# Kernel tuning notes

Hardware: AMD Instinct MI355X
Metric: run time of the kernel (lower is better)

## Reference

```python
import jax, jax.numpy as jnp
import numpy as np

B, SEQ, PRED, CIN, COUT = 4, 3584, 512, 7, 7
L = SEQ + PRED              # 4096, divisible by 2*BS -> fit_length is a no-op
D, H, DH, FF, EL = 512, 8, 64, 2048, 2
BS, NHASH = 64, 4           # bucket_size, n_hashes
NB = L // BS                # 64 buckets per hash round
SELF_ATTN_VAL = -5e4        # reformer_pytorch TOKEN_SELF_ATTN_VALUE


def layer_norm(x, g, b, eps=1e-5):
    m = jnp.mean(x, -1, keepdims=True)
    v = jnp.mean((x - m) ** 2, -1, keepdims=True)
    return (x - m) * jax.lax.rsqrt(v + eps) * g + b


def lsh_attention(qk, v, rot):
    # qk, v: (bh, L, DH); rot: (DH, NHASH, NB//2)  (shared across batch & heads)
    bh, Lx, dh = qk.shape
    nb = Lx // BS
    # --- hash vectors ---
    rv = jnp.einsum('btf,fhi->bhti', qk, rot)              # (bh, NHASH, L, nb//2)
    rv = jnp.concatenate([rv, -rv], axis=-1)
    buckets = jnp.argmax(rv, axis=-1)                      # (bh, NHASH, L) int
    buckets = buckets + (jnp.arange(NHASH) * nb)[None, :, None]
    buckets = buckets.reshape(bh, NHASH * Lx)
    ticker = jnp.arange(NHASH * Lx)
    bt = Lx * buckets + (ticker % Lx)[None]                # unique keys
    # --- sort by (bucket, position) ---
    sticker = jnp.argsort(bt, axis=-1)                     # (bh, NHASH*L)
    undo = jnp.argsort(sticker, axis=-1)
    st = sticker % Lx
    sqk = jnp.take_along_axis(qk, st[..., None], axis=1)   # (bh, NHASH*L, DH)
    sv = jnp.take_along_axis(v, st[..., None], axis=1)
    ch = NHASH * nb                                        # number of chunks
    bq_t = st.reshape(bh, ch, BS)
    bqk = sqk.reshape(bh, ch, BS, dh)
    bv = sv.reshape(bh, ch, BS, dh)
    bq = bqk
    nrm = jnp.sqrt(jnp.sum(bqk * bqk, -1, keepdims=True))
    bk = bqk / jnp.maximum(nrm, 1e-12)                     # F.normalize
    def look_one_back(t):
        prev = jnp.concatenate([t[:, -1:], t[:, :-1]], axis=1)
        return jnp.concatenate([t, prev], axis=2)
    bk = look_one_back(bk)
    bvv = look_one_back(bv)
    bkv_t = look_one_back(bq_t)
    dots = jnp.einsum('bcie,bcje->bcij', bq, bk) * (dh ** -0.5)  # (bh, ch, BS, 2BS)
    self_mask = bq_t[..., :, None] == bkv_t[..., None, :]
    dots = jnp.where(self_mask, SELF_ATTN_VAL, dots)
    lse = jax.scipy.special.logsumexp(dots, axis=-1, keepdims=True)
    p = jnp.exp(dots - lse)
    bo = jnp.einsum('bcij,bcje->bcie', p, bvv)
    so = bo.reshape(bh, NHASH * Lx, dh)
    slog = lse.reshape(bh, NHASH * Lx)
    o = jnp.take_along_axis(so, undo[..., None], axis=1)
    logits = jnp.take_along_axis(slog, undo, axis=1)
    o = o.reshape(bh, NHASH, Lx, dh)
    logits = logits.reshape(bh, NHASH, Lx, 1)
    probs = jnp.exp(logits - jax.scipy.special.logsumexp(logits, axis=1, keepdims=True))
    return jnp.sum(o * probs, axis=1)                      # (bh, L, DH)


def lsh_self_attention(x, Wqk, Wv, Wo, bo, rot):
    Bs, Lx, _ = x.shape
    qk = (x @ Wqk).reshape(Bs, Lx, H, DH).transpose(0, 2, 1, 3).reshape(Bs * H, Lx, DH)
    v = (x @ Wv).reshape(Bs, Lx, H, DH).transpose(0, 2, 1, 3).reshape(Bs * H, Lx, DH)
    out = lsh_attention(qk, v, rot)
    out = out.reshape(Bs, H, Lx, DH).transpose(0, 2, 1, 3).reshape(Bs, Lx, D)
    return out @ Wo + bo


def _forward(x_enc, x_dec, x_mark_enc, x_mark_dec, conv_w, month_emb, day_emb,
             weekday_emb, hour_emb, minute_emb, W_qk, W_v, W_out, b_out, rotations,
             ln1_g, ln1_b, W_ff1, b_ff1, W_ff2, b_ff2, ln2_g, ln2_b, lnf_g, lnf_b,
             W_proj, b_proj):
    x = jnp.concatenate([x_enc, x_dec[:, -PRED:, :]], axis=1)            # (B, L, CIN)
    xm = jnp.concatenate([x_mark_enc, x_mark_dec[:, -PRED:, :]], axis=1)
    # TokenEmbedding: Conv1d k=3, circular padding, no bias
    xp = jnp.concatenate([x[:, -1:], x, x[:, :1]], axis=1)
    tok = jax.lax.conv_general_dilated(xp, conv_w, (1,), 'VALID',
                                       dimension_numbers=('NWC', 'WIO', 'NWC'))
    # TemporalEmbedding (freq='t': month/day/weekday/hour/minute)
    temp = (month_emb[xm[..., 0]] + day_emb[xm[..., 1]] + weekday_emb[xm[..., 2]]
            + hour_emb[xm[..., 3]] + minute_emb[xm[..., 4]])
    # PositionalEmbedding (sinusoidal)
    pos = jnp.arange(L, dtype=jnp.float32)[:, None]
    div = jnp.exp(jnp.arange(0, D, 2, dtype=jnp.float32) * (-np.log(10000.0) / D))
    pe = jnp.zeros((L, D), jnp.float32).at[:, 0::2].set(jnp.sin(pos * div)).at[:, 1::2].set(jnp.cos(pos * div))
    h = tok + temp + pe[None]
    for l in range(EL):
        a = lsh_self_attention(h, W_qk[l], W_v[l], W_out[l], b_out[l], rotations[l])
        h = layer_norm(h + a, ln1_g[l], ln1_b[l])
        y = jax.nn.gelu(h @ W_ff1[l] + b_ff1[l], approximate=False)
        y = y @ W_ff2[l] + b_ff2[l]
        h = layer_norm(h + y, ln2_g[l], ln2_b[l])
    h = layer_norm(h, lnf_g, lnf_b)
    return h[:, -PRED:] @ W_proj + b_proj                  # (B, PRED, COUT)


def setup_inputs():
    ks = jax.random.split(jax.random.key(0), 20)
    def n(k, shape, fan_in):
        return jax.random.normal(k, shape, jnp.float32) / np.sqrt(fan_in)
    return {
        'x_enc': jax.random.normal(ks[0], (B, SEQ, CIN), jnp.float32),
        'x_dec': jax.random.normal(ks[1], (B, PRED, CIN), jnp.float32),
        'x_mark_enc': jax.random.randint(ks[2], (B, SEQ, 5), 0, 4, jnp.int32),
        'x_mark_dec': jax.random.randint(ks[3], (B, PRED, 5), 0, 4, jnp.int32),
        'conv_w': n(ks[4], (3, CIN, D), 3 * CIN),
        'month_emb': 0.02 * jax.random.normal(ks[5], (13, D), jnp.float32),
        'day_emb': 0.02 * jax.random.normal(ks[6], (32, D), jnp.float32),
        'weekday_emb': 0.02 * jax.random.normal(ks[7], (7, D), jnp.float32),
        'hour_emb': 0.02 * jax.random.normal(ks[8], (24, D), jnp.float32),
        'minute_emb': 0.02 * jax.random.normal(ks[9], (4, D), jnp.float32),
        'W_qk': n(ks[10], (EL, D, D), D),
        'W_v': n(ks[11], (EL, D, D), D),
        'W_out': n(ks[12], (EL, D, D), D),
        'b_out': jnp.zeros((EL, D), jnp.float32),
        'rotations': jax.random.normal(ks[13], (EL, DH, NHASH, NB // 2), jnp.float32),
        'ln1_g': jnp.ones((EL, D), jnp.float32),
        'ln1_b': jnp.zeros((EL, D), jnp.float32),
        'W_ff1': n(ks[14], (EL, D, FF), D),
        'b_ff1': jnp.zeros((EL, FF), jnp.float32),
        'W_ff2': n(ks[15], (EL, FF, D), FF),
        'b_ff2': jnp.zeros((EL, D), jnp.float32),
        'ln2_g': jnp.ones((EL, D), jnp.float32),
        'ln2_b': jnp.zeros((EL, D), jnp.float32),
        'lnf_g': jnp.ones((D,), jnp.float32),
        'lnf_b': jnp.zeros((D,), jnp.float32),
        'W_proj': n(ks[16], (D, COUT), D),
        'b_proj': jnp.zeros((COUT,), jnp.float32),
    }


def reference(x_enc, x_dec, x_mark_enc, x_mark_dec, conv_w, month_emb, day_emb,
              weekday_emb, hour_emb, minute_emb, W_qk, W_v, W_out, b_out, rotations,
              ln1_g, ln1_b, W_ff1, b_ff1, W_ff2, b_ff2, ln2_g, ln2_b, lnf_g, lnf_b,
              W_proj, b_proj):
    return _forward(x_enc, x_dec, x_mark_enc, x_mark_dec, conv_w, month_emb, day_emb,
                    weekday_emb, hour_emb, minute_emb, W_qk, W_v, W_out, b_out, rotations,
                    ln1_g, ln1_b, W_ff1, b_ff1, W_ff2, b_ff2, ln2_g, ln2_b, lnf_g, lnf_b,
                    W_proj, b_proj)
```

## Files before the change

kernel.cpp:

```cpp
#include <hip/hip_runtime.h>
#include <math.h>


typedef __attribute__((ext_vector_type(8))) __bf16 bf16x8;
typedef __attribute__((ext_vector_type(4))) float floatx4;

__device__ __forceinline__ unsigned short f2bf(float f) {
  union { float f; unsigned int u; } x; x.f = f;
  unsigned int r = x.u + 0x7fffu + ((x.u >> 16) & 1u);
  return (unsigned short)(r >> 16);
}
__device__ __forceinline__ float bf2f(unsigned short u) {
  union { unsigned int u; float f; } x; x.u = ((unsigned int)u) << 16;
  return x.f;
}
__device__ __forceinline__ float gelu_f(float x) {
  return 0.5f * x * (1.0f + erff(x * 0.70710678118654752440f));
}

__global__ __launch_bounds__(256) void pe_kernel(float* __restrict__ pe)
{
  int t = blockIdx.x;
#pragma unroll
  for (int rep = 0; rep < 2; ++rep) {
    int d = threadIdx.x + rep * 256;
    float cf = (float)(-9.210340371976184 / 512.0);
    float xf = (float)(d & ~1) * cf;
    float freq = (float)exp((double)xf);
    float angf = (float)t * freq;
    double a = (double)angf;
    pe[t * 512 + d] = (float)((d & 1) ? cos(a) : sin(a));
  }
}

__global__ __launch_bounds__(256) void embed_kernel(
    const float* __restrict__ x_enc, const float* __restrict__ x_dec,
    const int* __restrict__ xm_enc, const int* __restrict__ xm_dec,
    const float* __restrict__ conv_w,
    const float* __restrict__ month, const float* __restrict__ day,
    const float* __restrict__ wday, const float* __restrict__ hour,
    const float* __restrict__ minute, const float* __restrict__ pe,
    float* __restrict__ h)
{
  int idx = blockIdx.x;
  int b = idx >> 12, t = idx & 4095;
  __shared__ float xv[21];
  __shared__ int mi[5];
  int tid = threadIdx.x;
  if (tid < 21) {
    int w = tid / 7, c = tid % 7;
    int s = (t + w + 4095) & 4095;
    xv[tid] = (s < 3584) ? x_enc[(s + b*3584)*7 + c]
                         : x_dec[((s - 3584) + b*512)*7 + c];
  }
  if (tid >= 32 && tid < 37) {
    int j = tid - 32;
    mi[j] = (t < 3584) ? xm_enc[(b*3584 + t)*5 + j]
                       : xm_dec[(b*512 + (t - 3584))*5 + j];
  }
  __syncthreads();
  int m0 = mi[0], m1 = mi[1], m2 = mi[2], m3 = mi[3], m4 = mi[4];
#pragma unroll
  for (int rep = 0; rep < 2; ++rep) {
    int d = tid + rep*256;
    float tok = 0.f;
#pragma unroll
    for (int wc = 0; wc < 21; ++wc) tok += xv[wc] * conv_w[wc*512 + d];
    float temp = month[m0*512+d] + day[m1*512+d] + wday[m2*512+d]
               + hour[m3*512+d] + minute[m4*512+d];
    h[(size_t)idx*512 + d] = tok + temp + pe[t*512 + d];
  }
}

template<int ACT>
__global__ __launch_bounds__(256) void gemm_kernel(
    const float* __restrict__ A, const float* __restrict__ W,
    const float* __restrict__ bias, float* __restrict__ C,
    int M, int N, int K)
{
  __shared__ float As[8][132];
  __shared__ float Bs[8][132];
  int tid = threadIdx.x;
  int bm = blockIdx.x, bn = blockIdx.y;
  int tr = tid >> 4, tc = tid & 15;
  double acc[8][8];
  float tt[8][8];
#pragma unroll
  for (int i=0;i<8;++i)
#pragma unroll
    for (int j=0;j<8;++j) { acc[i][j]=0.0; tt[i][j]=0.f; }

  int am  = tid >> 1;
  int at  = (tid & 1) * 4;
  int bkr = tid >> 5;
  int bn4 = (tid & 31) * 4;
  const float* Aptr = A + (size_t)(bm*128 + am)*K + at;
  const float* Bptr = W + (size_t)bkr*N + bn*128 + bn4;

  int phase = 0;
  for (int k0 = 0; k0 < K; k0 += 8) {
    float4 a4 = *(const float4*)(Aptr + k0);
    float4 b4 = *(const float4*)(Bptr + (size_t)k0*N);
    __syncthreads();
    As[at+0][am] = a4.x; As[at+1][am] = a4.y;
    As[at+2][am] = a4.z; As[at+3][am] = a4.w;
    *(float4*)&Bs[bkr][bn4] = b4;
    __syncthreads();
#pragma unroll
    for (int k=0;k<8;++k) {
      float4 a0 = *(const float4*)&As[k][tr*8];
      float4 a1 = *(const float4*)&As[k][tr*8+4];
      float4 b0 = *(const float4*)&Bs[k][tc*8];
      float4 b1 = *(const float4*)&Bs[k][tc*8+4];
      float av[8] = {a0.x,a0.y,a0.z,a0.w,a1.x,a1.y,a1.z,a1.w};
      float bv[8] = {b0.x,b0.y,b0.z,b0.w,b1.x,b1.y,b1.z,b1.w};
#pragma unroll
      for (int i=0;i<8;++i)
#pragma unroll
        for (int j=0;j<8;++j) tt[i][j] += av[i]*bv[j];
    }
    phase ^= 1;
    if (!phase) {
#pragma unroll
      for (int i=0;i<8;++i)
#pragma unroll
        for (int j=0;j<8;++j) { acc[i][j] += (double)tt[i][j]; tt[i][j]=0.f; }
    }
  }
  int row0 = bm*128 + tr*8;
  int col0 = bn*128 + tc*8;
  float bvb[8];
#pragma unroll
  for (int j=0;j<8;++j) bvb[j] = bias ? bias[col0+j] : 0.f;
#pragma unroll
  for (int i=0;i<8;++i) {
    float o[8];
#pragma unroll
    for (int j=0;j<8;++j) {
      float vv = (float)acc[i][j] + bvb[j];
      if (ACT==1) vv = gelu_f(vv);
      o[j] = vv;
    }
    float4* dst = (float4*)(C + (size_t)(row0+i)*N + col0);
    dst[0] = make_float4(o[0],o[1],o[2],o[3]);
    dst[1] = make_float4(o[4],o[5],o[6],o[7]);
  }
}

template<int SPLIT>
__global__ __launch_bounds__(256) void wsplit_kernel(
    const float* __restrict__ W, unsigned short* __restrict__ Wt, int K, int N)
{
  __shared__ float tile[32][33];
  int k0 = blockIdx.x*32, n0 = blockIdx.y*32;
  int tid = threadIdx.x;
  int kk = tid >> 3, nn4 = (tid & 7)*4;
  float4 w4 = *(const float4*)(W + (size_t)(k0+kk)*N + n0 + nn4);
  tile[kk][nn4+0]=w4.x; tile[kk][nn4+1]=w4.y;
  tile[kk][nn4+2]=w4.z; tile[kk][nn4+3]=w4.w;
  __syncthreads();
  int n = tid >> 3, k4 = (tid & 7)*4;
  unsigned short o[3][4];
#pragma unroll
  for (int j=0;j<4;++j) {
    float v = tile[k4+j][n];
    unsigned short h0 = f2bf(v);
    float r = v - bf2f(h0);
    unsigned short h1 = f2bf(r);
    o[0][j] = h0; o[1][j] = h1;
    if (SPLIT==3) { float r2 = r - bf2f(h1); o[2][j] = f2bf(r2); }
  }
#pragma unroll
  for (int p=0;p<SPLIT;++p) {
    ushort4* d = (ushort4*)(Wt + (size_t)p*N*K + (size_t)(n0+n)*K + k0 + k4);
    *d = make_ushort4(o[p][0], o[p][1], o[p][2], o[p][3]);
  }
}

template<int SPLIT, int ACT>
__global__ __launch_bounds__(256, 3) void gemm_mfma(
    const float* __restrict__ A, const unsigned short* __restrict__ Wt,
    const float* __restrict__ bias, float* __restrict__ C,
    int M, int N, int K)
{
  constexpr int RS = SPLIT*32 + 8;
  __shared__ __align__(16) unsigned short smem[2*128*RS];
  unsigned short* sA = smem;
  unsigned short* sB = smem + 128*RS;
  float* sE = (float*)smem;

  int tid = threadIdx.x;
  int bm = blockIdx.x, bn = blockIdx.y;
  int lane = tid & 63, wave = tid >> 6;
  int wm = wave & 1, wn = wave >> 1;
  int fr = lane & 15, fk = (lane >> 4) * 8;

  floatx4 acc[4][4];
#pragma unroll
  for (int i=0;i<4;++i)
#pragma unroll
    for (int j=0;j<4;++j) acc[i][j] = (floatx4){0.f,0.f,0.f,0.f};

  int row = tid >> 1, kseg = (tid & 1) * 16;
  const float* aSrc = A + (size_t)(bm*128 + row)*K + kseg;
  const unsigned short* bSrc = Wt + (size_t)(bn*128 + row)*K + kseg;

  float4 av4[4];
  uint4 bv[SPLIT][2];
#pragma unroll
  for (int q=0;q<4;++q) av4[q] = *(const float4*)(aSrc + q*4);
#pragma unroll
  for (int p=0;p<SPLIT;++p) {
    const unsigned short* bp = bSrc + (size_t)p*N*K;
    bv[p][0] = *(const uint4*)(bp);
    bv[p][1] = *(const uint4*)(bp + 8);
  }

  for (int k0 = 0; k0 < K; k0 += 32) {
    __syncthreads();
    unsigned short us[SPLIT][16];
    const float* ff = (const float*)av4;
#pragma unroll
    for (int i=0;i<16;++i) {
      float v = ff[i];
      unsigned short h0 = f2bf(v);
      float r = v - bf2f(h0);
      us[0][i] = h0;
      unsigned short h1 = f2bf(r);
      us[1][i] = h1;
      if (SPLIT==3) { float r2 = r - bf2f(h1); us[2][i] = f2bf(r2); }
    }
#pragma unroll
    for (int p=0;p<SPLIT;++p) {
      uint4* d = (uint4*)&sA[row*RS + p*32 + kseg];
      d[0] = *(const uint4*)&us[p][0];
      d[1] = *(const uint4*)&us[p][8];
      uint4* db = (uint4*)&sB[row*RS + p*32 + kseg];
      db[0] = bv[p][0];
      db[1] = bv[p][1];
    }
    __syncthreads();
    if (k0 + 32 < K) {
#pragma unroll
      for (int q=0;q<4;++q) av4[q] = *(const float4*)(aSrc + k0 + 32 + q*4);
#pragma unroll
      for (int p=0;p<SPLIT;++p) {
        const unsigned short* bp = bSrc + (size_t)p*N*K + k0 + 32;
        bv[p][0] = *(const uint4*)(bp);
        bv[p][1] = *(const uint4*)(bp + 8);
      }
    }

    bf16x8 aF[4][SPLIT];
#pragma unroll
    for (int mt=0;mt<4;++mt)
#pragma unroll
      for (int p=0;p<SPLIT;++p)
        aF[mt][p] = *(const bf16x8*)&sA[(wm*64 + mt*16 + fr)*RS + p*32 + fk];
#pragma unroll
    for (int nt=0;nt<4;++nt) {
      bf16x8 bF[SPLIT];
#pragma unroll
      for (int p=0;p<SPLIT;++p)
        bF[p] = *(const bf16x8*)&sB[(wn*64 + nt*16 + fr)*RS + p*32 + fk];
#pragma unroll
      for (int mt=0;mt<4;++mt) {
        floatx4 c = acc[mt][nt];
        if (SPLIT==3) {
          c = __builtin_amdgcn_mfma_f32_16x16x32_bf16(aF[mt][2], bF[0], c, 0,0,0);
          c = __builtin_amdgcn_mfma_f32_16x16x32_bf16(aF[mt][1], bF[1], c, 0,0,0);
          c = __builtin_amdgcn_mfma_f32_16x16x32_bf16(aF[mt][0], bF[2], c, 0,0,0);
        }
        c = __builtin_amdgcn_mfma_f32_16x16x32_bf16(aF[mt][1], bF[0], c, 0,0,0);
        c = __builtin_amdgcn_mfma_f32_16x16x32_bf16(aF[mt][0], bF[1], c, 0,0,0);
        c = __builtin_amdgcn_mfma_f32_16x16x32_bf16(aF[mt][0], bF[0], c, 0,0,0);
        acc[mt][nt] = c;
      }
    }
  }

  __syncthreads();
#pragma unroll
  for (int half = 0; half < 2; ++half) {
    if (wm == half) {
#pragma unroll
      for (int nt=0;nt<4;++nt) {
        int cl = wn*64 + nt*16 + fr;
        float bb = bias ? bias[bn*128 + cl] : 0.f;
#pragma unroll
        for (int mt=0;mt<4;++mt) {
          int r0 = mt*16 + (lane>>4)*4;
#pragma unroll
          for (int j=0;j<4;++j) {
            float vv = acc[mt][nt][j] + bb;
            if (ACT==1) vv = gelu_f(vv);
            sE[(r0+j)*132 + cl] = vv;
          }
        }
      }
    }
    __syncthreads();
#pragma unroll
    for (int it=0; it<8; ++it) {
      int idx = it*256 + tid;
      int rr = idx >> 5, c4 = (idx & 31) * 4;
      float4 vv = *(const float4*)&sE[rr*132 + c4];
      *(float4*)(C + (size_t)(bm*128 + half*64 + rr)*N + bn*128 + c4) = vv;
    }
    __syncthreads();
  }
}

__global__ __launch_bounds__(256) void hash_kernel(
    const float* __restrict__ qk, const float* __restrict__ rot,
    unsigned char* __restrict__ buckets)
{
  __shared__ float q[2][64];
  __shared__ double rv[2][128];
  int half = threadIdx.x >> 7;
  int lt = threadIdx.x & 127;
  int g = blockIdx.x*2 + half;
  int bh = g >> 12, t = g & 4095;
  int b = bh >> 3, hd = bh & 7;
  if (lt < 64)
    q[half][lt] = qk[((size_t)(b*4096 + t))*512 + hd*64 + lt];
  __syncthreads();
  double acc = 0.0;
#pragma unroll 8
  for (int f=0; f<64; ++f) acc += (double)q[half][f] * (double)rot[f*128 + lt];
  rv[half][lt] = acc;
  __syncthreads();
  if (lt < 4) {
    const double* r = &rv[half][lt*32];
    double best = r[0]; int bi = 0;
#pragma unroll
    for (int j=1; j<64; ++j) {
      double v = (j < 32) ? r[j] : -r[j-32];
      if (v > best) { best = v; bi = j; }
    }
    buckets[((size_t)(bh*4 + lt))*4096 + t] = (unsigned char)bi;
  }
}

__global__ __launch_bounds__(64) void sort_kernel(
    const unsigned char* __restrict__ buckets, int* __restrict__ st)
{
  __shared__ unsigned char sb[4096];
  __shared__ int cnts[64];
  int tid = threadIdx.x;
  const unsigned int* src4 = (const unsigned int*)(buckets + (size_t)blockIdx.x*4096);
  unsigned int* sb4 = (unsigned int*)sb;
  for (int i=tid; i<1024; i+=64) sb4[i] = src4[i];
  __syncthreads();
  unsigned int me = (unsigned int)tid;
  int cnt = 0;
  for (int t4=0; t4<1024; ++t4) {
    unsigned int w = sb4[t4];
    cnt += ((w & 255u) == me) + (((w>>8)&255u) == me)
         + (((w>>16)&255u) == me) + ((w>>24) == me);
  }
  cnts[tid] = cnt;
  __syncthreads();
  int base = 0;
  for (int j=0;j<tid;++j) base += cnts[j];
  int* dst = st + (size_t)blockIdx.x*4096;
  for (int t4=0; t4<1024; ++t4) {
    unsigned int w = sb4[t4];
#pragma unroll
    for (int q=0;q<4;++q)
      if (((w >> (8*q)) & 255u) == me) dst[base++] = t4*4 + q;
  }
}

template<int SQ>
__global__ __launch_bounds__(256) void attn_mfma(
    const float* __restrict__ qk, const float* __restrict__ v,
    const int* __restrict__ st, float* __restrict__ osc,
    float* __restrict__ logits)
{
  constexpr int RQ = 72;
  constexpr int RP = 136;
  constexpr int QKE = SQ*128*RQ;
  constexpr int PVE = 2*64*RP*2;
  constexpr int UE = (QKE > PVE ? QKE : PVE);
  __shared__ __align__(16) unsigned short uni[UE];
  __shared__ int sPos[128];
  __shared__ float sInv[128];
  unsigned short* sQK = uni;
  unsigned short* sP  = uni;
  unsigned short* sVT = uni + 2*64*RP;

  int tid = threadIdx.x;
  int bh = blockIdx.x >> 8;
  int c  = blockIdx.x & 255;
  int b = bh >> 3, hd = bh & 7;
  int r = c >> 6;
  int lane = tid & 63, wave = tid >> 6;
  int fr = lane & 15, fq = lane >> 4;
  int fk = fq * 8;

  if (tid < 128) {
    int cprev = (c + 255) & 255;
    int slot = (tid < 64) ? (c*64 + tid) : (cprev*64 + tid - 64);
    sPos[tid] = st[bh*16384 + slot];
  }
  __syncthreads();

  int row = tid >> 1, ks2 = (tid & 1) * 32;
  float vreg[32];
  {
    size_t rbase = ((size_t)(b*4096 + sPos[row]))*512 + hd*64 + ks2;
    const float* src  = qk + rbase;
    const float* vsrc = v  + rbase;
    float qreg[32];
    float ss = 0.f;
#pragma unroll
    for (int i=0;i<32;i+=4) {
      float4 x = *(const float4*)(src + i);
      qreg[i]=x.x; qreg[i+1]=x.y; qreg[i+2]=x.z; qreg[i+3]=x.w;
      ss += x.x*x.x + x.y*x.y + x.z*x.z + x.w*x.w;
      float4 y = *(const float4*)(vsrc + i);
      vreg[i]=y.x; vreg[i+1]=y.y; vreg[i+2]=y.z; vreg[i+3]=y.w;
    }
    ss += __shfl_xor(ss, 1, 64);
    if ((tid & 1) == 0) sInv[row] = 1.0f / fmaxf(sqrtf(ss), 1e-12f);
    unsigned short us[3][32];
#pragma unroll
    for (int i=0;i<32;++i) {
      float vv = qreg[i];
      unsigned short h0 = f2bf(vv);
      float r1 = vv - bf2f(h0);
      unsigned short h1 = f2bf(r1);
      us[0][i] = h0; us[1][i] = h1;
      if (SQ==3) { float r2 = r1 - bf2f(h1); us[2][i] = f2bf(r2); }
    }
#pragma unroll
    for (int p=0;p<SQ;++p) {
      uint4* d = (uint4*)&sQK[p*128*RQ + row*RQ + ks2];
      d[0] = *(const uint4*)&us[p][0];
      d[1] = *(const uint4*)&us[p][8];
      d[2] = *(const uint4*)&us[p][16];
      d[3] = *(const uint4*)&us[p][24];
    }
  }
  __syncthreads();

  floatx4 s[8];
#pragma unroll
  for (int nt=0;nt<8;++nt) s[nt] = (floatx4){0.f,0.f,0.f,0.f};
#pragma unroll
  for (int ks=0; ks<2; ++ks) {
    bf16x8 aQ[SQ];
#pragma unroll
    for (int p=0;p<SQ;++p)
      aQ[p] = *(const bf16x8*)&sQK[p*128*RQ + (wave*16 + fr)*RQ + ks*32 + fk];
#pragma unroll
    for (int nt=0;nt<8;++nt) {
      bf16x8 bK[SQ];
#pragma unroll
      for (int p=0;p<SQ;++p)
        bK[p] = *(const bf16x8*)&sQK[p*128*RQ + (nt*16 + fr)*RQ + ks*32 + fk];
      floatx4 cc = s[nt];
      if (SQ==3) {
        cc = __builtin_amdgcn_mfma_f32_16x16x32_bf16(aQ[2], bK[0], cc, 0,0,0);
        cc = __builtin_amdgcn_mfma_f32_16x16x32_bf16(aQ[1], bK[1], cc, 0,0,0);
        cc = __builtin_amdgcn_mfma_f32_16x16x32_bf16(aQ[0], bK[2], cc, 0,0,0);
      }
      cc = __builtin_amdgcn_mfma_f32_16x16x32_bf16(aQ[1], bK[0], cc, 0,0,0);
      cc = __builtin_amdgcn_mfma_f32_16x16x32_bf16(aQ[0], bK[1], cc, 0,0,0);
      cc = __builtin_amdgcn_mfma_f32_16x16x32_bf16(aQ[0], bK[0], cc, 0,0,0);
      s[nt] = cc;
    }
  }

  int ipos[4];
#pragma unroll
  for (int reg=0;reg<4;++reg) ipos[reg] = sPos[wave*16 + fq*4 + reg];
  float dv[8][4];
  float mx[4] = {-1e30f,-1e30f,-1e30f,-1e30f};
#pragma unroll
  for (int nt=0;nt<8;++nt) {
    float invj = sInv[nt*16 + fr];
    int jpos = sPos[nt*16 + fr];
#pragma unroll
    for (int reg=0;reg<4;++reg) {
      float d = s[nt][reg] * invj * 0.125f;
      if (jpos == ipos[reg]) d = -5.0e4f;
      dv[nt][reg] = d;
      mx[reg] = fmaxf(mx[reg], d);
    }
  }
#pragma unroll
  for (int reg=0;reg<4;++reg) {
    mx[reg] = fmaxf(mx[reg], __shfl_xor(mx[reg], 1, 64));
    mx[reg] = fmaxf(mx[reg], __shfl_xor(mx[reg], 2, 64));
    mx[reg] = fmaxf(mx[reg], __shfl_xor(mx[reg], 4, 64));
    mx[reg] = fmaxf(mx[reg], __shfl_xor(mx[reg], 8, 64));
  }
  float sum[4] = {0.f,0.f,0.f,0.f};
#pragma unroll
  for (int nt=0;nt<8;++nt)
#pragma unroll
    for (int reg=0;reg<4;++reg) sum[reg] += expf(dv[nt][reg] - mx[reg]);
  float lse[4];
#pragma unroll
  for (int reg=0;reg<4;++reg) {
    sum[reg] += __shfl_xor(sum[reg], 1, 64);
    sum[reg] += __shfl_xor(sum[reg], 2, 64);
    sum[reg] += __shfl_xor(sum[reg], 4, 64);
    sum[reg] += __shfl_xor(sum[reg], 8, 64);
    lse[reg] = mx[reg] + logf(sum[reg]);
  }
  if (fr == 0) {
#pragma unroll
    for (int reg=0;reg<4;++reg)
      logits[((size_t)(bh*4 + r))*4096 + ipos[reg]] = lse[reg];
  }
#pragma unroll
  for (int nt=0;nt<8;++nt)
#pragma unroll
    for (int reg=0;reg<4;++reg) dv[nt][reg] = expf(dv[nt][reg] - lse[reg]);

  __syncthreads();

#pragma unroll
  for (int nt=0;nt<8;++nt) {
    int key = nt*16 + fr;
#pragma unroll
    for (int reg=0;reg<4;++reg) {
      int m = wave*16 + fq*4 + reg;
      float p = dv[nt][reg];
      unsigned short h0 = f2bf(p);
      sP[0*64*RP + m*RP + key] = h0;
      sP[1*64*RP + m*RP + key] = f2bf(p - bf2f(h0));
    }
  }
#pragma unroll
  for (int i=0;i<32;++i) {
    int dh = ks2 + i;
    float vv = vreg[i];
    unsigned short h0 = f2bf(vv);
    sVT[0*64*RP + dh*RP + row] = h0;
    sVT[1*64*RP + dh*RP + row] = f2bf(vv - bf2f(h0));
  }
  __syncthreads();

  size_t obase = ((size_t)(bh*4 + r)) * 4096;
#pragma unroll
  for (int dt=0;dt<4;++dt) {
    floatx4 o = (floatx4){0.f,0.f,0.f,0.f};
#pragma unroll
    for (int ks=0; ks<4; ++ks) {
      bf16x8 aP0 = *(const bf16x8*)&sP[0*64*RP + (wave*16 + fr)*RP + ks*32 + fk];
      bf16x8 aP1 = *(const bf16x8*)&sP[1*64*RP + (wave*16 + fr)*RP + ks*32 + fk];
      bf16x8 bV0 = *(const bf16x8*)&sVT[0*64*RP + (dt*16 + fr)*RP + ks*32 + fk];
      bf16x8 bV1 = *(const bf16x8*)&sVT[1*64*RP + (dt*16 + fr)*RP + ks*32 + fk];
      o = __builtin_amdgcn_mfma_f32_16x16x32_bf16(aP1, bV1, o, 0,0,0);
      o = __builtin_amdgcn_mfma_f32_16x16x32_bf16(aP1, bV0, o, 0,0,0);
      o = __builtin_amdgcn_mfma_f32_16x16x32_bf16(aP0, bV1, o, 0,0,0);
      o = __builtin_amdgcn_mfma_f32_16x16x32_bf16(aP0, bV0, o, 0,0,0);
    }
    int dh = dt*16 + fr;
#pragma unroll
    for (int reg=0;reg<4;++reg) {
      int m = wave*16 + fq*4 + reg;
      osc[(obase + sPos[m])*64 + dh] = o[reg];
    }
  }
}

__global__ __launch_bounds__(256) void combine_kernel(
    const float* __restrict__ osc, const float* __restrict__ logits,
    float* __restrict__ merged)
{
  int idx = blockIdx.x;
  int b = idx >> 12, t = idx & 4095;
  int tid = threadIdx.x;
  __shared__ float w[8][4];
  if (tid < 8) {
    size_t lbase = ((size_t)(b*8 + tid)) * 4 * 4096 + t;
    float l0 = logits[lbase], l1 = logits[lbase + 4096],
          l2 = logits[lbase + 8192], l3 = logits[lbase + 12288];
    float m = fmaxf(fmaxf(l0,l1), fmaxf(l2,l3));
    float e0 = expf(l0-m), e1 = expf(l1-m), e2 = expf(l2-m), e3 = expf(l3-m);
    float inv = 1.0f/(e0+e1+e2+e3);
    w[tid][0]=e0*inv; w[tid][1]=e1*inv; w[tid][2]=e2*inv; w[tid][3]=e3*inv;
  }
  __syncthreads();
#pragma unroll
  for (int rep=0; rep<2; ++rep) {
    int d = tid + rep*256;
    int hd = d >> 6, dh = d & 63;
    size_t obase = (((size_t)(b*8 + hd)) * 4 * 4096 + t) * 64 + dh;
    float o = w[hd][0]*osc[obase]
            + w[hd][1]*osc[obase + 262144]
            + w[hd][2]*osc[obase + 524288]
            + w[hd][3]*osc[obase + 786432];
    merged[(size_t)idx*512 + d] = o;
  }
}

__global__ __launch_bounds__(256) void ln_residual_kernel(
    float* __restrict__ h, const float* __restrict__ a,
    const float* __restrict__ g, const float* __restrict__ bb)
{
  int row = blockIdx.x;
  int tid = threadIdx.x;
  size_t base = (size_t)row * 512;
  float x0 = h[base + tid]       + a[base + tid];
  float x1 = h[base + tid + 256] + a[base + tid + 256];
  float s  = x0 + x1;
  float sq = x0*x0 + x1*x1;
#pragma unroll
  for (int off = 32; off > 0; off >>= 1) {
    s  += __shfl_down(s, off, 64);
    sq += __shfl_down(sq, off, 64);
  }
  __shared__ float rs[4], rq[4], sm[2];
  int wv = tid >> 6;
  if ((tid & 63) == 0) { rs[wv] = s; rq[wv] = sq; }
  __syncthreads();
  if (tid == 0) {
    float S = rs[0]+rs[1]+rs[2]+rs[3];
    float Q = rq[0]+rq[1]+rq[2]+rq[3];
    float m = S * (1.0f/512.0f);
    float var = Q * (1.0f/512.0f) - m*m;
    sm[0] = m; sm[1] = rsqrtf(var + 1e-5f);
  }
  __syncthreads();
  float m = sm[0], rstd = sm[1];
  h[base + tid]       = (x0 - m) * rstd * g[tid]       + bb[tid];
  h[base + tid + 256] = (x1 - m) * rstd * g[tid + 256] + bb[tid + 256];
}

__global__ __launch_bounds__(256) void final_kernel(
    const float* __restrict__ h, const float* __restrict__ g, const float* __restrict__ bb,
    const float* __restrict__ Wp, const float* __restrict__ bp, float* __restrict__ out)
{
  int idx = blockIdx.x;
  int b = idx >> 9, tp = idx & 511;
  size_t base = ((size_t)(b*4096 + 3584 + tp)) * 512;
  int tid = threadIdx.x;
  float x0 = h[base + tid], x1 = h[base + tid + 256];
  float s = x0 + x1, sq = x0*x0 + x1*x1;
#pragma unroll
  for (int off = 32; off > 0; off >>= 1) {
    s  += __shfl_down(s, off, 64);
    sq += __shfl_down(sq, off, 64);
  }
  __shared__ float rs[4], rq[4], sm[2];
  int wv = tid >> 6;
  if ((tid & 63) == 0) { rs[wv] = s; rq[wv] = sq; }
  __syncthreads();
  if (tid == 0) {
    float S = rs[0]+rs[1]+rs[2]+rs[3];
    float Q = rq[0]+rq[1]+rq[2]+rq[3];
    float m = S*(1.f/512.f);
    float var = Q*(1.f/512.f) - m*m;
    sm[0]=m; sm[1]=rsqrtf(var+1e-5f);
  }
  __syncthreads();
  __shared__ float xn[512];
  float m = sm[0], rstd = sm[1];
  xn[tid]     = (x0-m)*rstd*g[tid]     + bb[tid];
  xn[tid+256] = (x1-m)*rstd*g[tid+256] + bb[tid+256];
  __syncthreads();
  if (tid < 224) {
    int col = tid >> 5, lane = tid & 31;
    float p = 0.f;
    for (int f = lane; f < 512; f += 32) p += xn[f]*Wp[f*7 + col];
#pragma unroll
    for (int off=16; off>0; off>>=1) p += __shfl_down(p, off, 32);
    if (lane == 0) out[(size_t)idx*7 + col] = p + bp[col];
  }
}

extern "C" void kernel_launch(void* const* d_in, const int* in_sizes, int n_in,
                              void* d_out, int out_size, void* d_ws, size_t ws_size,
                              hipStream_t stream)
{
  (void)in_sizes; (void)n_in; (void)out_size; (void)ws_size;
  const float* x_enc  = (const float*)d_in[0];
  const float* x_dec  = (const float*)d_in[1];
  const int*   xm_enc = (const int*)d_in[2];
  const int*   xm_dec = (const int*)d_in[3];
  const float* conv_w = (const float*)d_in[4];
  const float* month  = (const float*)d_in[5];
  const float* day    = (const float*)d_in[6];
  const float* wday   = (const float*)d_in[7];
  const float* hourE  = (const float*)d_in[8];
  const float* minE   = (const float*)d_in[9];
  const float* W_qk   = (const float*)d_in[10];
  const float* W_v    = (const float*)d_in[11];
  const float* W_out  = (const float*)d_in[12];
  const float* b_out  = (const float*)d_in[13];
  const float* rots   = (const float*)d_in[14];
  const float* ln1_g  = (const float*)d_in[15];
  const float* ln1_b  = (const float*)d_in[16];
  const float* W_ff1  = (const float*)d_in[17];
  const float* b_ff1  = (const float*)d_in[18];
  const float* W_ff2  = (const float*)d_in[19];
  const float* b_ff2  = (const float*)d_in[20];
  const float* ln2_g  = (const float*)d_in[21];
  const float* ln2_b  = (const float*)d_in[22];
  const float* lnf_g  = (const float*)d_in[23];
  const float* lnf_b  = (const float*)d_in[24];
  const float* W_proj = (const float*)d_in[25];
  const float* b_proj = (const float*)d_in[26];

  float* h    = (float*)d_ws;
  float* bufA = h    + 8388608ull;
  float* bufB = bufA + 8388608ull;
  float* osc  = bufB + 8388608ull;
  float* lg   = osc  + 33554432ull;
  int*   stp  = (int*)(lg + 524288ull);
  unsigned char* bkt = (unsigned char*)(stp + 524288ull);
  float* pe   = osc;
  unsigned short* WtA = (unsigned short*)osc;
  unsigned short* WtB = (unsigned short*)bufB;

  pe_kernel<<<4096, 256, 0, stream>>>(pe);
  embed_kernel<<<16384, 256, 0, stream>>>(x_enc, x_dec, xm_enc, xm_dec, conv_w,
                                          month, day, wday, hourE, minE, pe, h);
  for (int l = 0; l < 2; ++l) {
    const float* Wqk = W_qk + (size_t)l*262144;
    const float* Wv  = W_v  + (size_t)l*262144;
    const float* Wo  = W_out+ (size_t)l*262144;
    const float* Wf1 = W_ff1 + (size_t)l*1048576;
    const float* Wf2 = W_ff2 + (size_t)l*1048576;
    const float* rot = rots + (size_t)l*8192;

    gemm_kernel<0><<<dim3(128,4), 256, 0, stream>>>(h, Wqk, nullptr, bufA, 16384, 512, 512);
    if (l == 0) {
      wsplit_kernel<3><<<dim3(16,16), 256, 0, stream>>>(Wv, WtA, 512, 512);
      gemm_mfma<3,0><<<dim3(128,4), 256, 0, stream>>>(h, WtA, nullptr, bufB, 16384, 512, 512);
    } else {
      wsplit_kernel<2><<<dim3(16,16), 256, 0, stream>>>(Wv, WtA, 512, 512);
      gemm_mfma<2,0><<<dim3(128,4), 256, 0, stream>>>(h, WtA, nullptr, bufB, 16384, 512, 512);
    }
    hash_kernel<<<65536, 256, 0, stream>>>(bufA, rot, bkt);
    sort_kernel<<<128, 64, 0, stream>>>(bkt, stp);
    if (l == 0)
      attn_mfma<3><<<8192, 256, 0, stream>>>(bufA, bufB, stp, osc, lg);
    else
      attn_mfma<2><<<8192, 256, 0, stream>>>(bufA, bufB, stp, osc, lg);
    combine_kernel<<<16384, 256, 0, stream>>>(osc, lg, bufA);
    if (l == 0) {
      wsplit_kernel<3><<<dim3(16,16), 256, 0, stream>>>(Wo, WtA, 512, 512);
      gemm_mfma<3,0><<<dim3(128,4), 256, 0, stream>>>(bufA, WtA, b_out + l*512, bufB, 16384, 512, 512);
    } else {
      wsplit_kernel<2><<<dim3(16,16), 256, 0, stream>>>(Wo, WtA, 512, 512);
      gemm_mfma<2,0><<<dim3(128,4), 256, 0, stream>>>(bufA, WtA, b_out + l*512, bufB, 16384, 512, 512);
    }
    ln_residual_kernel<<<16384, 256, 0, stream>>>(h, bufB, ln1_g + l*512, ln1_b + l*512);
    if (l == 0) {
      wsplit_kernel<3><<<dim3(16,64), 256, 0, stream>>>(Wf1, WtB, 512, 2048);
      gemm_mfma<3,1><<<dim3(128,16), 256, 0, stream>>>(h, WtB, b_ff1 + l*2048, osc, 16384, 2048, 512);
      wsplit_kernel<3><<<dim3(64,16), 256, 0, stream>>>(Wf2, WtB, 2048, 512);
      gemm_mfma<3,0><<<dim3(128,4), 256, 0, stream>>>(osc, WtB, b_ff2 + l*512, bufA, 16384, 512, 2048);
    } else {
      wsplit_kernel<2><<<dim3(16,64), 256, 0, stream>>>(Wf1, WtB, 512, 2048);
      gemm_mfma<2,1><<<dim3(128,16), 256, 0, stream>>>(h, WtB, b_ff1 + l*2048, osc, 16384, 2048, 512);
      wsplit_kernel<2><<<dim3(64,16), 256, 0, stream>>>(Wf2, WtB, 2048, 512);
      gemm_mfma<2,0><<<dim3(128,4), 256, 0, stream>>>(osc, WtB, b_ff2 + l*512, bufA, 16384, 512, 2048);
    }
    ln_residual_kernel<<<16384, 256, 0, stream>>>(h, bufA, ln2_g + l*512, ln2_b + l*512);
  }
  final_kernel<<<2048, 256, 0, stream>>>(h, lnf_g, lnf_b, W_proj, b_proj, (float*)d_out);
}
```

Baseline: 3.342 ms.

## Use 256x128 block tiles for feed-forward split-bf16 MFMA GEMMs

Adds a GEMM variant where each block computes a 256x128 output tile instead of 128x128, with each wave holding 8x4 MFMA accumulator tiles. The FF1 and FF2 GEMMs now use it with half as many blocks along M. The goal is more reuse of each loaded and split B tile, and fewer per-block float-to-bf16 conversions of weights. In exchange it uses more registers (128 accumulator floats per lane) and more LDS, runs fewer blocks, and writes the epilogue out in four passes.

```diff
diff --git a/kernel.cpp b/kernel.cpp
--- a/kernel.cpp
+++ b/kernel.cpp
@@ -306,6 +306,158 @@
       int rr = idx >> 5, c4 = (idx & 31) * 4;
       float4 vv = *(const float4*)&sE[rr*132 + c4];
       *(float4*)(C + (size_t)(bm*128 + half*64 + rr)*N + bn*128 + c4) = vv;
+    }
+    __syncthreads();
+  }
+}
+
+template<int SPLIT, int ACT>
+__global__ __launch_bounds__(256, 2) void gemm_mfma256(
+    const float* __restrict__ A, const unsigned short* __restrict__ Wt,
+    const float* __restrict__ bias, float* __restrict__ C,
+    int M, int N, int K)
+{
+  constexpr int RS = SPLIT*32 + 8;
+  __shared__ __align__(16) unsigned short smem[384*RS];
+  unsigned short* sA = smem;
+  unsigned short* sB = smem + 256*RS;
+  float* sE = (float*)smem;
+
+  int tid = threadIdx.x;
+  int bm = blockIdx.x, bn = blockIdx.y;
+  int lane = tid & 63, wave = tid >> 6;
+  int wm = wave & 1, wn = wave >> 1;
+  int fr = lane & 15, fk = (lane >> 4) * 8;
+
+  floatx4 acc[8][4];
+#pragma unroll
+  for (int i=0;i<8;++i)
+#pragma unroll
+    for (int j=0;j<4;++j) acc[i][j] = (floatx4){0.f,0.f,0.f,0.f};
+
+  int row = tid >> 1, kseg = (tid & 1) * 16;
+  const float* aSrc0 = A + (size_t)(bm*256 + row)*K + kseg;
+  const float* aSrc1 = A + (size_t)(bm*256 + 128 + row)*K + kseg;
+  const unsigned short* bSrc = Wt + (size_t)(bn*128 + row)*K + kseg;
+
+  float4 av4[2][4];
+  uint4 bv[SPLIT][2];
+#pragma unroll
+  for (int q=0;q<4;++q) {
+    av4[0][q] = *(const float4*)(aSrc0 + q*4);
+    av4[1][q] = *(const float4*)(aSrc1 + q*4);
+  }
+#pragma unroll
+  for (int p=0;p<SPLIT;++p) {
+    const unsigned short* bp = bSrc + (size_t)p*N*K;
+    bv[p][0] = *(const uint4*)(bp);
+    bv[p][1] = *(const uint4*)(bp + 8);
+  }
+
+  for (int k0 = 0; k0 < K; k0 += 32) {
+    __syncthreads();
+#pragma unroll
+    for (int r2 = 0; r2 < 2; ++r2) {
+      unsigned short us[SPLIT][16];
+      const float* ff = (const float*)av4[r2];
+#pragma unroll
+      for (int i=0;i<16;++i) {
+        float v = ff[i];
+        unsigned short h0 = f2bf(v);
+        float r = v - bf2f(h0);
+        us[0][i] = h0;
+        unsigned short h1 = f2bf(r);
+        us[1][i] = h1;
+        if (SPLIT==3) { float r2r = r - bf2f(h1); us[2][i] = f2bf(r2r); }
+      }
+#pragma unroll
+      for (int p=0;p<SPLIT;++p) {
+        uint4* d = (uint4*)&sA[(r2*128 + row)*RS + p*32 + kseg];
+        d[0] = *(const uint4*)&us[p][0];
+        d[1] = *(const uint4*)&us[p][8];
+      }
+    }
+#pragma unroll
+    for (int p=0;p<SPLIT;++p) {
+      uint4* db = (uint4*)&sB[row*RS + p*32 + kseg];
+      db[0] = bv[p][0];
+      db[1] = bv[p][1];
+    }
+    __syncthreads();
+    if (k0 + 32 < K) {
+#pragma unroll
+      for (int q=0;q<4;++q) {
+        av4[0][q] = *(const float4*)(aSrc0 + k0 + 32 + q*4);
+        av4[1][q] = *(const float4*)(aSrc1 + k0 + 32 + q*4);
+      }
+#pragma unroll
+      for (int p=0;p<SPLIT;++p) {
+        const unsigned short* bp = bSrc + (size_t)p*N*K + k0 + 32;
+        bv[p][0] = *(const uint4*)(bp);
+        bv[p][1] = *(const uint4*)(bp + 8);
+      }
+    }
+
+#pragma unroll
+    for (int np = 0; np < 2; ++np) {
+      bf16x8 bF[2][SPLIT];
+#pragma unroll
+      for (int n2=0;n2<2;++n2)
+#pragma unroll
+        for (int p=0;p<SPLIT;++p)
+          bF[n2][p] = *(const bf16x8*)&sB[(wn*64 + (np*2+n2)*16 + fr)*RS + p*32 + fk];
+#pragma unroll
+      for (int mt=0; mt<8; ++mt) {
+        bf16x8 aF[SPLIT];
+#pragma unroll
+        for (int p=0;p<SPLIT;++p)
+          aF[p] = *(const bf16x8*)&sA[(wm*128 + mt*16 + fr)*RS + p*32 + fk];
+#pragma unroll
+        for (int n2=0;n2<2;++n2) {
+          int nt = np*2 + n2;
+          floatx4 c = acc[mt][nt];
+          if (SPLIT==3) {
+            c = __builtin_amdgcn_mfma_f32_16x16x32_bf16(aF[2], bF[n2][0], c, 0,0,0);
+            c = __builtin_amdgcn_mfma_f32_16x16x32_bf16(aF[1], bF[n2][1], c, 0,0,0);
+            c = __builtin_amdgcn_mfma_f32_16x16x32_bf16(aF[0], bF[n2][2], c, 0,0,0);
+          }
+          c = __builtin_amdgcn_mfma_f32_16x16x32_bf16(aF[1], bF[n2][0], c, 0,0,0);
+          c = __builtin_amdgcn_mfma_f32_16x16x32_bf16(aF[0], bF[n2][1], c, 0,0,0);
+          c = __builtin_amdgcn_mfma_f32_16x16x32_bf16(aF[0], bF[n2][0], c, 0,0,0);
+          acc[mt][nt] = c;
+        }
+      }
+    }
+  }
+
+  __syncthreads();
+#pragma unroll
+  for (int q = 0; q < 4; ++q) {
+    if (wm == (q >> 1)) {
+#pragma unroll
+      for (int nt=0;nt<4;++nt) {
+        int cl = wn*64 + nt*16 + fr;
+        float bb = bias ? bias[bn*128 + cl] : 0.f;
+#pragma unroll
+        for (int mtl=0;mtl<4;++mtl) {
+          int mt = (q & 1)*4 + mtl;
+          int r0 = mtl*16 + (lane>>4)*4;
+#pragma unroll
+          for (int j=0;j<4;++j) {
+            float vv = acc[mt][nt][j] + bb;
+            if (ACT==1) vv = gelu_f(vv);
+            sE[(r0+j)*132 + cl] = vv;
+          }
+        }
+      }
+    }
+    __syncthreads();
+#pragma unroll
+    for (int it=0; it<8; ++it) {
+      int idx = it*256 + tid;
+      int rr = idx >> 5, c4 = (idx & 31) * 4;
+      float4 vv = *(const float4*)&sE[rr*132 + c4];
+      *(float4*)(C + (size_t)(bm*256 + q*64 + rr)*N + bn*128 + c4) = vv;
     }
     __syncthreads();
   }
@@ -755,14 +907,14 @@
     ln_residual_kernel<<<16384, 256, 0, stream>>>(h, bufB, ln1_g + l*512, ln1_b + l*512);
     if (l == 0) {
       wsplit_kernel<3><<<dim3(16,64), 256, 0, stream>>>(Wf1, WtB, 512, 2048);
-      gemm_mfma<3,1><<<dim3(128,16), 256, 0, stream>>>(h, WtB, b_ff1 + l*2048, osc, 16384, 2048, 512);
+      gemm_mfma256<3,1><<<dim3(64,16), 256, 0, stream>>>(h, WtB, b_ff1 + l*2048, osc, 16384, 2048, 512);
       wsplit_kernel<3><<<dim3(64,16), 256, 0, stream>>>(Wf2, WtB, 2048, 512);
-      gemm_mfma<3,0><<<dim3(128,4), 256, 0, stream>>>(osc, WtB, b_ff2 + l*512, bufA, 16384, 512, 2048);
+      gemm_mfma256<3,0><<<dim3(64,4), 256, 0, stream>>>(osc, WtB, b_ff2 + l*512, bufA, 16384, 512, 2048);
     } else {
       wsplit_kernel<2><<<dim3(16,64), 256, 0, stream>>>(Wf1, WtB, 512, 2048);
-      gemm_mfma<2,1><<<dim3(128,16), 256, 0, stream>>>(h, WtB, b_ff1 + l*2048, osc, 16384, 2048, 512);
+      gemm_mfma256<2,1><<<dim3(64,16), 256, 0, stream>>>(h, WtB, b_ff1 + l*2048, osc, 16384, 2048, 512);
       wsplit_kernel<2><<<dim3(64,16), 256, 0, stream>>>(Wf2, WtB, 2048, 512);
-      gemm_mfma<2,0><<<dim3(128,4), 256, 0, stream>>>(osc, WtB, b_ff2 + l*512, bufA, 16384, 512, 2048);
+      gemm_mfma256<2,0><<<dim3(64,4), 256, 0, stream>>>(osc, WtB, b_ff2 + l*512, bufA, 16384, 512, 2048);
     }
     ln_residual_kernel<<<16384, 256, 0, stream>>>(h, bufA, ln2_g + l*512, ln2_b + l*512);
   }
```

Measured after the change: 3.643 ms. 9.0% more time.
